# Kernel optimization log

Measured on AMD Instinct MI355X. Metric: run time of the kernel, lower is better.

Reference implementation:

```python
import jax, jax.numpy as jnp
import numpy as np

EPS = 1e-12  # matches torch.nn.functional.normalize default eps


def _l2norm(x, axis=-1):
    # F.normalize: x / max(||x||, eps)
    n = jnp.sqrt(jnp.sum(x * x, axis=axis, keepdims=True))
    return x / jnp.maximum(n, EPS)


def setup_inputs() -> dict:
    key = jax.random.key(0)
    k1, k2, k3 = jax.random.split(key, 3)
    batch, n_mels, time_steps = 32, 80, 4000
    num_codebooks, codebook_size, d = 2, 1024, 64
    mel = jax.random.normal(k1, (batch, n_mels, time_steps), dtype=jnp.float32)
    proj = jax.random.normal(k2, (num_codebooks, n_mels, d), dtype=jnp.float32)
    codebooks = jax.random.normal(k3, (num_codebooks, codebook_size, d), dtype=jnp.float32)
    return {"mel": mel, "proj": proj, "codebooks": codebooks}


def reference(mel, proj, codebooks):
    # mel: [b, n, t] -> [b, t, n]
    mel_t = jnp.transpose(mel, (0, 2, 1))
    # project for all codebooks at once: [c, b, t, d]
    p = jnp.einsum('btn,cnd->cbtd', mel_t, proj)
    p = _l2norm(p, axis=-1)
    cb = _l2norm(codebooks, axis=-1)  # [c, k, d]
    # cosine similarity: [c, b, t, k]
    sim = jnp.einsum('cbtd,ckd->cbtk', p, cb)
    codes = jnp.argmax(sim, axis=-1)  # [c, b, t]
    return codes
```

## Files before the change

kernel.cpp:

```cpp
#include <hip/hip_runtime.h>
#include <hip/hip_bf16.h>
#include <math.h>
#include <stdint.h>


#define B      32
#define NMELS  80
#define TSTEPS 4000
#define NCB    2
#define KCB    1024
#define DDIM   64
#define TPB    256
#define TM     64
#define KT     32
#define NKT    (KCB / KT)
#define PPAD   66

typedef short bf16x8 __attribute__((ext_vector_type(8)));
typedef float f32x4  __attribute__((ext_vector_type(4)));

#define WS_CB_OFF   8192
#define WS_NEEDED   (8192 + NCB*KCB*DDIM*2)

static __device__ __forceinline__ uint32_t bits(float f) {
    return __builtin_bit_cast(uint32_t, f);
}
static __device__ __forceinline__ float fbits(uint32_t u) {
    return __builtin_bit_cast(float, u);
}
static __device__ __forceinline__ uint32_t rne16(uint32_t u) {
    return (u + 0x7FFFu + ((u >> 16) & 1u)) >> 16;
}

__global__ __launch_bounds__(TPB) void rpq_prep(const float* __restrict__ cb,
                                                float* __restrict__ ws)
{
    const int idx = blockIdx.x * TPB + threadIdx.x;
    if (idx >= NCB * KCB) return;

    const float4* row = (const float4*)(cb + (size_t)idx * DDIM);
    float4 v[16];
    float ss = 0.f;
    #pragma unroll
    for (int i = 0; i < 16; ++i) {
        v[i] = row[i];
        ss += v[i].x*v[i].x + v[i].y*v[i].y + v[i].z*v[i].z + v[i].w*v[i].w;
    }
    const float inv = 1.0f / fmaxf(sqrtf(ss), 1e-12f);
    ws[idx] = inv;

    uint32_t dw[32];
    #pragma unroll
    for (int i = 0; i < 16; ++i) {
        dw[2*i]   = rne16(bits(v[i].x * inv)) | (rne16(bits(v[i].y * inv)) << 16);
        dw[2*i+1] = rne16(bits(v[i].z * inv)) | (rne16(bits(v[i].w * inv)) << 16);
    }
    uint4* dst = (uint4*)((char*)ws + WS_CB_OFF + (size_t)idx * 128);
    #pragma unroll
    for (int i = 0; i < 8; ++i)
        dst[i] = make_uint4(dw[4*i], dw[4*i+1], dw[4*i+2], dw[4*i+3]);
}

__global__ __launch_bounds__(TPB, 5) void rpq_main(
    const float* __restrict__ mel,
    const float* __restrict__ proj,
    const float* __restrict__ cb,
    const float* __restrict__ ws,
    int* __restrict__ out)
{
    const int tid  = threadIdx.x;
    const int b    = blockIdx.y;
    const int c    = blockIdx.z;
    const int t0   = blockIdx.x * TM;

    const int l    = tid & 63;
    const int wid  = tid >> 6;
    const int lrow = l & 15;
    const int lgrp = l >> 4;

    __shared__ union __align__(16) {
        float projS[NMELS * DDIM];
        struct {
            union {
                char     cbuf[2][KT * 128];
                uint32_t candT[16][TM][2];
            } a;
            float PL[TM * PPAD];
            float scv[TM][9];
            int   sck[TM][9];
        } p2;
    } U;

    const char*  wscb   = (const char*)ws + WS_CB_OFF + (size_t)c * (KCB * 128);
    const float* invn_g = ws + (size_t)c * KCB;

    {
        const float4* src = (const float4*)(proj + (size_t)c * NMELS * DDIM);
        float4* dst = (float4*)U.projS;
        for (int i = tid; i < NMELS * DDIM / 4; i += TPB) dst[i] = src[i];
    }
    __syncthreads();

    const int srow = tid >> 3;
    const int sq   = tid & 7;
    uint4 g0;
    g0 = *(const uint4*)(wscb + (size_t)tid * 16);

    {
        const int tq = tid & 15;
        const int dg = tid >> 4;
        const int tbase  = t0 + tq * 4;
        const int tb_c   = (tbase <= TSTEPS - 4) ? tbase : (TSTEPS - 4);
        const float* mp  = mel + (size_t)b * NMELS * TSTEPS + tb_c;

        float Pa[4][4];
        #pragma unroll
        for (int i = 0; i < 4; ++i)
            #pragma unroll
            for (int j = 0; j < 4; ++j) Pa[i][j] = 0.f;

        for (int n = 0; n < NMELS; ++n) {
            const float4 m4 = *(const float4*)(mp + (size_t)n * TSTEPS);
            const float4 w  = *(const float4*)&U.projS[n * DDIM + dg * 4];
            Pa[0][0] = fmaf(m4.x, w.x, Pa[0][0]); Pa[0][1] = fmaf(m4.x, w.y, Pa[0][1]);
            Pa[0][2] = fmaf(m4.x, w.z, Pa[0][2]); Pa[0][3] = fmaf(m4.x, w.w, Pa[0][3]);
            Pa[1][0] = fmaf(m4.y, w.x, Pa[1][0]); Pa[1][1] = fmaf(m4.y, w.y, Pa[1][1]);
            Pa[1][2] = fmaf(m4.y, w.z, Pa[1][2]); Pa[1][3] = fmaf(m4.y, w.w, Pa[1][3]);
            Pa[2][0] = fmaf(m4.z, w.x, Pa[2][0]); Pa[2][1] = fmaf(m4.z, w.y, Pa[2][1]);
            Pa[2][2] = fmaf(m4.z, w.z, Pa[2][2]); Pa[2][3] = fmaf(m4.z, w.w, Pa[2][3]);
            Pa[3][0] = fmaf(m4.w, w.x, Pa[3][0]); Pa[3][1] = fmaf(m4.w, w.y, Pa[3][1]);
            Pa[3][2] = fmaf(m4.w, w.z, Pa[3][2]); Pa[3][3] = fmaf(m4.w, w.w, Pa[3][3]);
        }
        __syncthreads();

        #pragma unroll
        for (int i = 0; i < 4; ++i)
            *(float4*)&U.p2.PL[(tq * 4 + i) * PPAD + dg * 4] =
                make_float4(Pa[i][0], Pa[i][1], Pa[i][2], Pa[i][3]);
    }

    {
        const int xw = (srow & 7) << 4;
        *(uint4*)(&U.p2.a.cbuf[0][srow * 128] + ((sq * 16) ^ xw)) = g0;
    }
    __syncthreads();

    bf16x8 A0, A1;
    {
        const float* pr = &U.p2.PL[((wid << 4) + lrow) * PPAD];
        #pragma unroll
        for (int i = 0; i < 8; ++i) {
            A0[i] = (short)rne16(bits(pr[lgrp * 8 + i]));
            A1[i] = (short)rne16(bits(pr[32 + lgrp * 8 + i]));
        }
    }

    float m1[4], m2[4];
    #pragma unroll
    for (int r = 0; r < 4; ++r) { m1[r] = -INFINITY; m2[r] = -INFINITY; }
    uint32_t idxv = (uint32_t)(1023 - lrow);

    const int xr  = (lrow & 7) << 4;
    const int bo0 = (lgrp * 16) ^ xr;
    const int bo1 = (64 + lgrp * 16) ^ xr;

    for (int kt = 0; kt < NKT; ++kt) {
        const int cur = kt & 1;
        if (kt + 1 < NKT) {
            g0 = *(const uint4*)(wscb + (size_t)(kt + 1) * (KT * 128)
                                 + (size_t)tid * 16);
        }
        const char* buf = U.p2.a.cbuf[cur];
        #pragma unroll
        for (int s = 0; s < 2; ++s) {
            const char* rowp = buf + (s * 16 + lrow) * 128;
            bf16x8 B0 = *(const bf16x8*)(rowp + bo0);
            bf16x8 B1 = *(const bf16x8*)(rowp + bo1);
            f32x4 acc = {0.f, 0.f, 0.f, 0.f};
            acc = __builtin_amdgcn_mfma_f32_16x16x32_bf16(A0, B0, acc, 0, 0, 0);
            acc = __builtin_amdgcn_mfma_f32_16x16x32_bf16(A1, B1, acc, 0, 0, 0);
            #pragma unroll
            for (int r = 0; r < 4; ++r) {
                const float pf = fbits((bits(acc[r]) & 0xFFFFFC00u)
                                     | (idxv & 0x3FFu));
                m2[r] = __builtin_amdgcn_fmed3f(pf, m1[r], m2[r]);
                m1[r] = fmaxf(pf, m1[r]);
            }
            idxv -= 16u;
        }
        if (kt + 1 < NKT) {
            const int xw = (srow & 7) << 4;
            *(uint4*)(&U.p2.a.cbuf[cur ^ 1][srow * 128] + ((sq * 16) ^ xw)) = g0;
        }
        __syncthreads();
    }

    #pragma unroll
    for (int r = 0; r < 4; ++r) {
        const int trow = (wid << 4) + (lgrp << 2) + r;
        U.p2.a.candT[lrow][trow][0] = bits(m1[r]);
        U.p2.a.candT[lrow][trow][1] = bits(m2[r]);
    }
    __syncthreads();

    {
        const int t = tid & 63;
        const int j = wid;
        float c1 = -INFINITY, c2 = -INFINITY, c3 = -INFINITY, c4 = -INFINITY;
        float c5 = -INFINITY, c6 = -INFINITY, c7 = -INFINITY, c8 = -INFINITY;
        for (int i = 0; i < 16; ++i) {
            const uint2 pv2 = *(const uint2*)&U.p2.a.candT[i][t][0];
            #pragma unroll
            for (int jj = 0; jj < 2; ++jj) {
                const float p = fbits(jj ? pv2.y : pv2.x);
                c8 = fmaxf(fminf(p, c7), c8);
                c7 = fmaxf(fminf(p, c6), c7);
                c6 = fmaxf(fminf(p, c5), c6);
                c5 = fmaxf(fminf(p, c4), c5);
                c4 = fmaxf(fminf(p, c3), c4);
                c3 = fmaxf(fminf(p, c2), c3);
                c2 = fmaxf(fminf(p, c1), c2);
                c1 = fmaxf(p, c1);
            }
        }
        const float sel0 = (j == 0) ? c1 : (j == 1) ? c3 : (j == 2) ? c5 : c7;
        const float sel1 = (j == 0) ? c2 : (j == 1) ? c4 : (j == 2) ? c6 : c8;
        const float* pr  = &U.p2.PL[t * PPAD];
        const float* cbc = cb + (size_t)c * KCB * DDIM;
        #pragma unroll
        for (int e = 0; e < 2; ++e) {
            const float sel = e ? sel1 : sel0;
            const int kj = 1023 - (int)(bits(sel) & 0x3FFu);
            const float* cbr = cbc + (size_t)kj * DDIM;
            float a0 = 0.f, a1 = 0.f, a2 = 0.f, a3 = 0.f;
            #pragma unroll
            for (int i = 0; i < 16; ++i) {
                float4 pv = *(const float4*)(pr + i * 4);
                float4 cv = *(const float4*)(cbr + i * 4);
                a0 = fmaf(pv.x, cv.x, a0); a1 = fmaf(pv.y, cv.y, a1);
                a2 = fmaf(pv.z, cv.z, a2); a3 = fmaf(pv.w, cv.w, a3);
            }
            U.p2.scv[t][2*j + e] = ((a0 + a1) + (a2 + a3)) * invn_g[kj];
            U.p2.sck[t][2*j + e] = kj;
        }
    }
    __syncthreads();

    if (tid < TM) {
        const int tg = t0 + tid;
        if (tg < TSTEPS) {
            float best = U.p2.scv[tid][0];
            int   bk   = U.p2.sck[tid][0];
            #pragma unroll
            for (int s2 = 1; s2 < 8; ++s2) {
                const float v = U.p2.scv[tid][s2];
                const int  kk = U.p2.sck[tid][s2];
                if (v > best || (v == best && kk < bk)) { best = v; bk = kk; }
            }
            out[((size_t)c * B + b) * TSTEPS + tg] = bk;
        }
    }
}

__global__ __launch_bounds__(TPB, 2) void rpq_fallback(
    const float* __restrict__ mel, const float* __restrict__ proj,
    const float* __restrict__ cb, int* __restrict__ out)
{
    const int tid = threadIdx.x;
    const int b = blockIdx.y, c = blockIdx.z;
    const int t0 = blockIdx.x * (TPB * 2) + tid;
    const int t1 = t0 + TPB;
    const int tc0 = (t0 < TSTEPS) ? t0 : (TSTEPS - 1);
    const int tc1 = (t1 < TSTEPS) ? t1 : (TSTEPS - 1);

    __shared__ union { float projS[NMELS*DDIM]; float cbS[2][64*DDIM]; } sh;
    __shared__ float invn[KCB];
    const float* cbc = cb + (size_t)c * KCB * DDIM;
    {
        const float4* src = (const float4*)(proj + (size_t)c * NMELS * DDIM);
        float4* dst = (float4*)sh.projS;
        for (int i = tid; i < NMELS*DDIM/4; i += TPB) dst[i] = src[i];
    }
    for (int j = 0; j < KCB/TPB; ++j) {
        const int k = j*TPB + tid;
        const float4* r = (const float4*)(cbc + (size_t)k * DDIM);
        float s = 0.f;
        #pragma unroll
        for (int i = 0; i < DDIM/4; ++i) {
            float4 v = r[i]; s += v.x*v.x + v.y*v.y + v.z*v.z + v.w*v.w;
        }
        invn[k] = 1.0f / fmaxf(sqrtf(s), 1e-12f);
    }
    float4 r0, r1, r2, r3;
    { const float4* g = (const float4*)cbc;
      r0 = g[tid]; r1 = g[tid+256]; r2 = g[tid+512]; r3 = g[tid+768]; }
    __syncthreads();
    float P0[DDIM], P1[DDIM];
    #pragma unroll
    for (int d = 0; d < DDIM; ++d) { P0[d] = 0.f; P1[d] = 0.f; }
    const float* mp = mel + (size_t)b * NMELS * TSTEPS;
    for (int n = 0; n < NMELS; ++n) {
        const float m0 = mp[(size_t)n*TSTEPS + tc0];
        const float m1_ = mp[(size_t)n*TSTEPS + tc1];
        const float4* ps = (const float4*)(sh.projS + n*DDIM);
        #pragma unroll
        for (int i = 0; i < DDIM/4; ++i) {
            float4 v = ps[i];
            P0[4*i+0]=fmaf(m0,v.x,P0[4*i+0]); P0[4*i+1]=fmaf(m0,v.y,P0[4*i+1]);
            P0[4*i+2]=fmaf(m0,v.z,P0[4*i+2]); P0[4*i+3]=fmaf(m0,v.w,P0[4*i+3]);
            P1[4*i+0]=fmaf(m1_,v.x,P1[4*i+0]); P1[4*i+1]=fmaf(m1_,v.y,P1[4*i+1]);
            P1[4*i+2]=fmaf(m1_,v.z,P1[4*i+2]); P1[4*i+3]=fmaf(m1_,v.w,P1[4*i+3]);
        }
    }
    __syncthreads();
    { float4* dst = (float4*)sh.cbS[0];
      dst[tid]=r0; dst[tid+256]=r1; dst[tid+512]=r2; dst[tid+768]=r3; }
    { const float4* g = (const float4*)(cbc + (size_t)64*DDIM);
      r0=g[tid]; r1=g[tid+256]; r2=g[tid+512]; r3=g[tid+768]; }
    __syncthreads();
    float best0 = -INFINITY, best1 = -INFINITY; int bi0 = 0, bi1 = 0;
    for (int kt = 0; kt < KCB/64; ++kt) {
        const int cur = kt & 1;
        const float* base = sh.cbS[cur];
        const int kbase = kt * 64;
        #pragma unroll 2
        for (int kk = 0; kk < 64; ++kk) {
            const float4* row = (const float4*)(base + kk*DDIM);
            float a0=0,a1=0,a2=0,a3=0,b0=0,b1=0,b2=0,b3=0;
            #pragma unroll
            for (int i = 0; i < DDIM/4; ++i) {
                float4 v = row[i];
                a0=fmaf(P0[4*i+0],v.x,a0); a1=fmaf(P0[4*i+1],v.y,a1);
                a2=fmaf(P0[4*i+2],v.z,a2); a3=fmaf(P0[4*i+3],v.w,a3);
                b0=fmaf(P1[4*i+0],v.x,b0); b1=fmaf(P1[4*i+1],v.y,b1);
                b2=fmaf(P1[4*i+2],v.z,b2); b3=fmaf(P1[4*i+3],v.w,b3);
            }
            const int k = kbase + kk;
            const float w = invn[k];
            const float s0 = ((a0+a1)+(a2+a3))*w;
            const float s1 = ((b0+b1)+(b2+b3))*w;
            if (s0 > best0) { best0 = s0; bi0 = k; }
            if (s1 > best1) { best1 = s1; bi1 = k; }
        }
        if (kt + 1 < KCB/64) {
            float4* dst = (float4*)sh.cbS[cur ^ 1];
            dst[tid]=r0; dst[tid+256]=r1; dst[tid+512]=r2; dst[tid+768]=r3;
            if (kt + 2 < KCB/64) {
                const float4* g = (const float4*)(cbc + (size_t)(kt+2)*64*DDIM);
                r0=g[tid]; r1=g[tid+256]; r2=g[tid+512]; r3=g[tid+768];
            }
        }
        __syncthreads();
    }
    const size_t ob = ((size_t)c * B + b) * TSTEPS;
    if (t0 < TSTEPS) out[ob + t0] = bi0;
    if (t1 < TSTEPS) out[ob + t1] = bi1;
}

extern "C" void kernel_launch(void* const* d_in, const int* in_sizes, int n_in,
                              void* d_out, int out_size, void* d_ws, size_t ws_size,
                              hipStream_t stream) {
    const float* mel  = (const float*)d_in[0];
    const float* proj = (const float*)d_in[1];
    const float* cb   = (const float*)d_in[2];
    int* out = (int*)d_out;

    if (ws_size >= (size_t)WS_NEEDED) {
        float* ws = (float*)d_ws;
        rpq_prep<<<dim3((NCB*KCB + TPB - 1)/TPB), dim3(TPB), 0, stream>>>(cb, ws);
        dim3 grid((TSTEPS + TM - 1) / TM, B, NCB);
        rpq_main<<<grid, dim3(TPB), 0, stream>>>(mel, proj, cb, ws, out);
    } else {
        dim3 grid((TSTEPS + TPB*2 - 1) / (TPB*2), B, NCB);
        rpq_fallback<<<grid, dim3(TPB), 0, stream>>>(mel, proj, cb, out);
    }
}
```

Measured before the change: 193.1 us.

## Split codebook across waves, reading B directly from global without LDS staging

Each wave now processes all 64 time rows against its own quarter of the codebook (256 entries), loading bf16 codebook fragments straight from global/L2 instead of double-buffering them through LDS with a block barrier every tile. Per-lane top-2 candidates are merged with xor-shuffles within the wave and written once per wave, replacing the 16-way shared-memory candidate transpose and the serial top-8 insertion. This removes the per-tile __syncthreads and LDS traffic and reuses each B fragment across four A tiles. In exchange it raises register pressure (4 A tiles, 16 m1/m2 pairs), so occupancy drops to 4 blocks, and B loads now depend on global latency.

```diff
diff --git a/kernel.cpp b/kernel.cpp
--- a/kernel.cpp
+++ b/kernel.cpp
@@ -12,8 +12,6 @@
 #define DDIM   64
 #define TPB    256
 #define TM     64
-#define KT     32
-#define NKT    (KCB / KT)
 #define PPAD   66
 
 typedef short bf16x8 __attribute__((ext_vector_type(8)));
@@ -61,7 +59,7 @@
         dst[i] = make_uint4(dw[4*i], dw[4*i+1], dw[4*i+2], dw[4*i+3]);
 }
 
-__global__ __launch_bounds__(TPB, 5) void rpq_main(
+__global__ __launch_bounds__(TPB, 4) void rpq_main(
     const float* __restrict__ mel,
     const float* __restrict__ proj,
     const float* __restrict__ cb,
@@ -81,11 +79,8 @@
     __shared__ union __align__(16) {
         float projS[NMELS * DDIM];
         struct {
-            union {
-                char     cbuf[2][KT * 128];
-                uint32_t candT[16][TM][2];
-            } a;
             float PL[TM * PPAD];
+            uint2 wcand[4][TM];
             float scv[TM][9];
             int   sck[TM][9];
         } p2;
@@ -100,11 +95,6 @@
         for (int i = tid; i < NMELS * DDIM / 4; i += TPB) dst[i] = src[i];
     }
     __syncthreads();
-
-    const int srow = tid >> 3;
-    const int sq   = tid & 7;
-    uint4 g0;
-    g0 = *(const uint4*)(wscb + (size_t)tid * 16);
 
     {
         const int tq = tid & 15;
@@ -138,99 +128,80 @@
             *(float4*)&U.p2.PL[(tq * 4 + i) * PPAD + dg * 4] =
                 make_float4(Pa[i][0], Pa[i][1], Pa[i][2], Pa[i][3]);
     }
-
-    {
-        const int xw = (srow & 7) << 4;
-        *(uint4*)(&U.p2.a.cbuf[0][srow * 128] + ((sq * 16) ^ xw)) = g0;
-    }
-    __syncthreads();
-
-    bf16x8 A0, A1;
-    {
-        const float* pr = &U.p2.PL[((wid << 4) + lrow) * PPAD];
+    __syncthreads();
+
+    bf16x8 A0[4], A1[4];
+    #pragma unroll
+    for (int tb = 0; tb < 4; ++tb) {
+        const float* pr = &U.p2.PL[(tb * 16 + lrow) * PPAD];
         #pragma unroll
         for (int i = 0; i < 8; ++i) {
-            A0[i] = (short)rne16(bits(pr[lgrp * 8 + i]));
-            A1[i] = (short)rne16(bits(pr[32 + lgrp * 8 + i]));
-        }
-    }
-
-    float m1[4], m2[4];
-    #pragma unroll
-    for (int r = 0; r < 4; ++r) { m1[r] = -INFINITY; m2[r] = -INFINITY; }
-    uint32_t idxv = (uint32_t)(1023 - lrow);
-
-    const int xr  = (lrow & 7) << 4;
-    const int bo0 = (lgrp * 16) ^ xr;
-    const int bo1 = (64 + lgrp * 16) ^ xr;
-
-    for (int kt = 0; kt < NKT; ++kt) {
-        const int cur = kt & 1;
-        if (kt + 1 < NKT) {
-            g0 = *(const uint4*)(wscb + (size_t)(kt + 1) * (KT * 128)
-                                 + (size_t)tid * 16);
-        }
-        const char* buf = U.p2.a.cbuf[cur];
-        #pragma unroll
-        for (int s = 0; s < 2; ++s) {
-            const char* rowp = buf + (s * 16 + lrow) * 128;
-            bf16x8 B0 = *(const bf16x8*)(rowp + bo0);
-            bf16x8 B1 = *(const bf16x8*)(rowp + bo1);
+            A0[tb][i] = (short)rne16(bits(pr[lgrp * 8 + i]));
+            A1[tb][i] = (short)rne16(bits(pr[32 + lgrp * 8 + i]));
+        }
+    }
+
+    float m1[4][4], m2[4][4];
+    #pragma unroll
+    for (int tb = 0; tb < 4; ++tb)
+        #pragma unroll
+        for (int r = 0; r < 4; ++r) { m1[tb][r] = -INFINITY; m2[tb][r] = -INFINITY; }
+
+    const char* qbase = wscb + (size_t)wid * (256 * 128);
+    const int lo0 = lrow * 128 + lgrp * 16;
+    const int lo1 = lo0 + 64;
+    uint32_t idxv = (uint32_t)(1023 - (wid << 8) - lrow);
+
+    #pragma unroll 4
+    for (int g = 0; g < 16; ++g) {
+        const bf16x8 B0 = *(const bf16x8*)(qbase + g * 2048 + lo0);
+        const bf16x8 B1 = *(const bf16x8*)(qbase + g * 2048 + lo1);
+        #pragma unroll
+        for (int tb = 0; tb < 4; ++tb) {
             f32x4 acc = {0.f, 0.f, 0.f, 0.f};
-            acc = __builtin_amdgcn_mfma_f32_16x16x32_bf16(A0, B0, acc, 0, 0, 0);
-            acc = __builtin_amdgcn_mfma_f32_16x16x32_bf16(A1, B1, acc, 0, 0, 0);
+            acc = __builtin_amdgcn_mfma_f32_16x16x32_bf16(A0[tb], B0, acc, 0, 0, 0);
+            acc = __builtin_amdgcn_mfma_f32_16x16x32_bf16(A1[tb], B1, acc, 0, 0, 0);
             #pragma unroll
             for (int r = 0; r < 4; ++r) {
                 const float pf = fbits((bits(acc[r]) & 0xFFFFFC00u)
                                      | (idxv & 0x3FFu));
-                m2[r] = __builtin_amdgcn_fmed3f(pf, m1[r], m2[r]);
-                m1[r] = fmaxf(pf, m1[r]);
-            }
-            idxv -= 16u;
-        }
-        if (kt + 1 < NKT) {
-            const int xw = (srow & 7) << 4;
-            *(uint4*)(&U.p2.a.cbuf[cur ^ 1][srow * 128] + ((sq * 16) ^ xw)) = g0;
-        }
-        __syncthreads();
-    }
-
-    #pragma unroll
-    for (int r = 0; r < 4; ++r) {
-        const int trow = (wid << 4) + (lgrp << 2) + r;
-        U.p2.a.candT[lrow][trow][0] = bits(m1[r]);
-        U.p2.a.candT[lrow][trow][1] = bits(m2[r]);
+                m2[tb][r] = __builtin_amdgcn_fmed3f(pf, m1[tb][r], m2[tb][r]);
+                m1[tb][r] = fmaxf(pf, m1[tb][r]);
+            }
+        }
+        idxv -= 16u;
+    }
+
+    #pragma unroll
+    for (int tb = 0; tb < 4; ++tb) {
+        #pragma unroll
+        for (int r = 0; r < 4; ++r) {
+            float a1 = m1[tb][r], a2 = m2[tb][r];
+            #pragma unroll
+            for (int m = 1; m <= 8; m <<= 1) {
+                const float b1 = __shfl_xor(a1, m);
+                const float b2 = __shfl_xor(a2, m);
+                const float lo = fminf(a1, b1);
+                a1 = fmaxf(a1, b1);
+                a2 = fmaxf(lo, fmaxf(a2, b2));
+            }
+            if (lrow == 0)
+                U.p2.wcand[wid][tb * 16 + (lgrp << 2) + r] =
+                    make_uint2(bits(a1), bits(a2));
+        }
     }
     __syncthreads();
 
     {
         const int t = tid & 63;
         const int j = wid;
-        float c1 = -INFINITY, c2 = -INFINITY, c3 = -INFINITY, c4 = -INFINITY;
-        float c5 = -INFINITY, c6 = -INFINITY, c7 = -INFINITY, c8 = -INFINITY;
-        for (int i = 0; i < 16; ++i) {
-            const uint2 pv2 = *(const uint2*)&U.p2.a.candT[i][t][0];
-            #pragma unroll
-            for (int jj = 0; jj < 2; ++jj) {
-                const float p = fbits(jj ? pv2.y : pv2.x);
-                c8 = fmaxf(fminf(p, c7), c8);
-                c7 = fmaxf(fminf(p, c6), c7);
-                c6 = fmaxf(fminf(p, c5), c6);
-                c5 = fmaxf(fminf(p, c4), c5);
-                c4 = fmaxf(fminf(p, c3), c4);
-                c3 = fmaxf(fminf(p, c2), c3);
-                c2 = fmaxf(fminf(p, c1), c2);
-                c1 = fmaxf(p, c1);
-            }
-        }
-        const float sel0 = (j == 0) ? c1 : (j == 1) ? c3 : (j == 2) ? c5 : c7;
-        const float sel1 = (j == 0) ? c2 : (j == 1) ? c4 : (j == 2) ? c6 : c8;
+        const uint2 cd = U.p2.wcand[j][t];
         const float* pr  = &U.p2.PL[t * PPAD];
         const float* cbc = cb + (size_t)c * KCB * DDIM;
         #pragma unroll
         for (int e = 0; e < 2; ++e) {
-            const float sel = e ? sel1 : sel0;
-            const int kj = 1023 - (int)(bits(sel) & 0x3FFu);
+            const uint32_t sv = e ? cd.y : cd.x;
+            const int kj = 1023 - (int)(sv & 0x3FFu);
             const float* cbr = cbc + (size_t)kj * DDIM;
             float a0 = 0.f, a1 = 0.f, a2 = 0.f, a3 = 0.f;
             #pragma unroll
```

Result: faster. 177.9 us (-7.9%).

## Stream bf16 codebook directly from global memory with smaller wave-local blocks

Applied to the files above, without the earlier changes.

The main kernel drops LDS staging of both the projection matrix and the bf16 codebook tiles. Projection weights are read straight from global memory, and each wave loads its MFMA B operands from the prepped workspace with no per-tile barriers. Blocks shrink to 128 threads covering 32 time steps with higher occupancy bounds, and candidate reduction becomes per-wave. This removes LDS traffic and __syncthreads in the codebook loop, but relies on L1/L2 caching for repeated codebook and projection reads across many more blocks.

```diff
diff --git a/kernel.cpp b/kernel.cpp
--- a/kernel.cpp
+++ b/kernel.cpp
@@ -10,10 +10,8 @@
 #define NCB    2
 #define KCB    1024
 #define DDIM   64
-#define TPB    256
-#define TM     64
-#define KT     32
-#define NKT    (KCB / KT)
+#define TPB    128
+#define TM     32
 #define PPAD   66
 
 typedef short bf16x8 __attribute__((ext_vector_type(8)));
@@ -32,10 +30,10 @@
     return (u + 0x7FFFu + ((u >> 16) & 1u)) >> 16;
 }
 
-__global__ __launch_bounds__(TPB) void rpq_prep(const float* __restrict__ cb,
+__global__ __launch_bounds__(256) void rpq_prep(const float* __restrict__ cb,
                                                 float* __restrict__ ws)
 {
-    const int idx = blockIdx.x * TPB + threadIdx.x;
+    const int idx = blockIdx.x * 256 + threadIdx.x;
     if (idx >= NCB * KCB) return;
 
     const float4* row = (const float4*)(cb + (size_t)idx * DDIM);
@@ -61,7 +59,7 @@
         dst[i] = make_uint4(dw[4*i], dw[4*i+1], dw[4*i+2], dw[4*i+3]);
 }
 
-__global__ __launch_bounds__(TPB, 5) void rpq_main(
+__global__ __launch_bounds__(TPB, 8) void rpq_main(
     const float* __restrict__ mel,
     const float* __restrict__ proj,
     const float* __restrict__ cb,
@@ -74,44 +72,25 @@
     const int t0   = blockIdx.x * TM;
 
     const int l    = tid & 63;
-    const int wid  = tid >> 6;
+    const int w    = tid >> 6;
     const int lrow = l & 15;
     const int lgrp = l >> 4;
 
-    __shared__ union __align__(16) {
-        float projS[NMELS * DDIM];
-        struct {
-            union {
-                char     cbuf[2][KT * 128];
-                uint32_t candT[16][TM][2];
-            } a;
-            float PL[TM * PPAD];
-            float scv[TM][9];
-            int   sck[TM][9];
-        } p2;
-    } U;
+    __shared__ struct __align__(16) {
+        float    PL[TM * PPAD];
+        uint2    cand[2][16][17];
+        float    scv[2][16][9];
+        int      sck[2][16][9];
+    } S;
 
     const char*  wscb   = (const char*)ws + WS_CB_OFF + (size_t)c * (KCB * 128);
     const float* invn_g = ws + (size_t)c * KCB;
 
     {
-        const float4* src = (const float4*)(proj + (size_t)c * NMELS * DDIM);
-        float4* dst = (float4*)U.projS;
-        for (int i = tid; i < NMELS * DDIM / 4; i += TPB) dst[i] = src[i];
-    }
-    __syncthreads();
-
-    const int srow = tid >> 3;
-    const int sq   = tid & 7;
-    uint4 g0;
-    g0 = *(const uint4*)(wscb + (size_t)tid * 16);
-
-    {
-        const int tq = tid & 15;
-        const int dg = tid >> 4;
-        const int tbase  = t0 + tq * 4;
-        const int tb_c   = (tbase <= TSTEPS - 4) ? tbase : (TSTEPS - 4);
-        const float* mp  = mel + (size_t)b * NMELS * TSTEPS + tb_c;
+        const int tq = tid & 7;
+        const int dg = tid >> 3;
+        const float* mp = mel + (size_t)b * NMELS * TSTEPS + t0 + tq * 4;
+        const float* pj = proj + (size_t)c * NMELS * DDIM + dg * 4;
 
         float Pa[4][4];
         #pragma unroll
@@ -121,33 +100,26 @@
 
         for (int n = 0; n < NMELS; ++n) {
             const float4 m4 = *(const float4*)(mp + (size_t)n * TSTEPS);
-            const float4 w  = *(const float4*)&U.projS[n * DDIM + dg * 4];
-            Pa[0][0] = fmaf(m4.x, w.x, Pa[0][0]); Pa[0][1] = fmaf(m4.x, w.y, Pa[0][1]);
-            Pa[0][2] = fmaf(m4.x, w.z, Pa[0][2]); Pa[0][3] = fmaf(m4.x, w.w, Pa[0][3]);
-            Pa[1][0] = fmaf(m4.y, w.x, Pa[1][0]); Pa[1][1] = fmaf(m4.y, w.y, Pa[1][1]);
-            Pa[1][2] = fmaf(m4.y, w.z, Pa[1][2]); Pa[1][3] = fmaf(m4.y, w.w, Pa[1][3]);
-            Pa[2][0] = fmaf(m4.z, w.x, Pa[2][0]); Pa[2][1] = fmaf(m4.z, w.y, Pa[2][1]);
-            Pa[2][2] = fmaf(m4.z, w.z, Pa[2][2]); Pa[2][3] = fmaf(m4.z, w.w, Pa[2][3]);
-            Pa[3][0] = fmaf(m4.w, w.x, Pa[3][0]); Pa[3][1] = fmaf(m4.w, w.y, Pa[3][1]);
-            Pa[3][2] = fmaf(m4.w, w.z, Pa[3][2]); Pa[3][3] = fmaf(m4.w, w.w, Pa[3][3]);
-        }
-        __syncthreads();
-
+            const float4 wv = *(const float4*)(pj + (size_t)n * DDIM);
+            Pa[0][0] = fmaf(m4.x, wv.x, Pa[0][0]); Pa[0][1] = fmaf(m4.x, wv.y, Pa[0][1]);
+            Pa[0][2] = fmaf(m4.x, wv.z, Pa[0][2]); Pa[0][3] = fmaf(m4.x, wv.w, Pa[0][3]);
+            Pa[1][0] = fmaf(m4.y, wv.x, Pa[1][0]); Pa[1][1] = fmaf(m4.y, wv.y, Pa[1][1]);
+            Pa[1][2] = fmaf(m4.y, wv.z, Pa[1][2]); Pa[1][3] = fmaf(m4.y, wv.w, Pa[1][3]);
+            Pa[2][0] = fmaf(m4.z, wv.x, Pa[2][0]); Pa[2][1] = fmaf(m4.z, wv.y, Pa[2][1]);
+            Pa[2][2] = fmaf(m4.z, wv.z, Pa[2][2]); Pa[2][3] = fmaf(m4.z, wv.w, Pa[2][3]);
+            Pa[3][0] = fmaf(m4.w, wv.x, Pa[3][0]); Pa[3][1] = fmaf(m4.w, wv.y, Pa[3][1]);
+            Pa[3][2] = fmaf(m4.w, wv.z, Pa[3][2]); Pa[3][3] = fmaf(m4.w, wv.w, Pa[3][3]);
+        }
         #pragma unroll
         for (int i = 0; i < 4; ++i)
-            *(float4*)&U.p2.PL[(tq * 4 + i) * PPAD + dg * 4] =
+            *(float4*)&S.PL[(tq * 4 + i) * PPAD + dg * 4] =
                 make_float4(Pa[i][0], Pa[i][1], Pa[i][2], Pa[i][3]);
-    }
-
-    {
-        const int xw = (srow & 7) << 4;
-        *(uint4*)(&U.p2.a.cbuf[0][srow * 128] + ((sq * 16) ^ xw)) = g0;
     }
     __syncthreads();
 
     bf16x8 A0, A1;
     {
-        const float* pr = &U.p2.PL[((wid << 4) + lrow) * PPAD];
+        const float* pr = &S.PL[(w * 16 + lrow) * PPAD];
         #pragma unroll
         for (int i = 0; i < 8; ++i) {
             A0[i] = (short)rne16(bits(pr[lgrp * 8 + i]));
@@ -158,58 +130,39 @@
     float m1[4], m2[4];
     #pragma unroll
     for (int r = 0; r < 4; ++r) { m1[r] = -INFINITY; m2[r] = -INFINITY; }
+
+    const int lo0 = lrow * 128 + lgrp * 16;
+    const int lo1 = lo0 + 64;
     uint32_t idxv = (uint32_t)(1023 - lrow);
 
-    const int xr  = (lrow & 7) << 4;
-    const int bo0 = (lgrp * 16) ^ xr;
-    const int bo1 = (64 + lgrp * 16) ^ xr;
-
-    for (int kt = 0; kt < NKT; ++kt) {
-        const int cur = kt & 1;
-        if (kt + 1 < NKT) {
-            g0 = *(const uint4*)(wscb + (size_t)(kt + 1) * (KT * 128)
-                                 + (size_t)tid * 16);
-        }
-        const char* buf = U.p2.a.cbuf[cur];
-        #pragma unroll
-        for (int s = 0; s < 2; ++s) {
-            const char* rowp = buf + (s * 16 + lrow) * 128;
-            bf16x8 B0 = *(const bf16x8*)(rowp + bo0);
-            bf16x8 B1 = *(const bf16x8*)(rowp + bo1);
-            f32x4 acc = {0.f, 0.f, 0.f, 0.f};
-            acc = __builtin_amdgcn_mfma_f32_16x16x32_bf16(A0, B0, acc, 0, 0, 0);
-            acc = __builtin_amdgcn_mfma_f32_16x16x32_bf16(A1, B1, acc, 0, 0, 0);
-            #pragma unroll
-            for (int r = 0; r < 4; ++r) {
-                const float pf = fbits((bits(acc[r]) & 0xFFFFFC00u)
-                                     | (idxv & 0x3FFu));
-                m2[r] = __builtin_amdgcn_fmed3f(pf, m1[r], m2[r]);
-                m1[r] = fmaxf(pf, m1[r]);
-            }
-            idxv -= 16u;
-        }
-        if (kt + 1 < NKT) {
-            const int xw = (srow & 7) << 4;
-            *(uint4*)(&U.p2.a.cbuf[cur ^ 1][srow * 128] + ((sq * 16) ^ xw)) = g0;
-        }
-        __syncthreads();
-    }
-
-    #pragma unroll
-    for (int r = 0; r < 4; ++r) {
-        const int trow = (wid << 4) + (lgrp << 2) + r;
-        U.p2.a.candT[lrow][trow][0] = bits(m1[r]);
-        U.p2.a.candT[lrow][trow][1] = bits(m2[r]);
-    }
+    #pragma unroll 4
+    for (int g = 0; g < 64; ++g) {
+        const bf16x8 B0 = *(const bf16x8*)(wscb + (size_t)g * 2048 + lo0);
+        const bf16x8 B1 = *(const bf16x8*)(wscb + (size_t)g * 2048 + lo1);
+        f32x4 acc = {0.f, 0.f, 0.f, 0.f};
+        acc = __builtin_amdgcn_mfma_f32_16x16x32_bf16(A0, B0, acc, 0, 0, 0);
+        acc = __builtin_amdgcn_mfma_f32_16x16x32_bf16(A1, B1, acc, 0, 0, 0);
+        #pragma unroll
+        for (int r = 0; r < 4; ++r) {
+            const float pf = fbits((bits(acc[r]) & 0xFFFFFC00u) | (idxv & 0x3FFu));
+            m2[r] = __builtin_amdgcn_fmed3f(pf, m1[r], m2[r]);
+            m1[r] = fmaxf(pf, m1[r]);
+        }
+        idxv -= 16u;
+    }
+
+    #pragma unroll
+    for (int r = 0; r < 4; ++r)
+        S.cand[w][(lgrp << 2) + r][lrow] = make_uint2(bits(m1[r]), bits(m2[r]));
     __syncthreads();
 
     {
-        const int t = tid & 63;
-        const int j = wid;
+        const int t = l & 15;
+        const int j = lgrp;
         float c1 = -INFINITY, c2 = -INFINITY, c3 = -INFINITY, c4 = -INFINITY;
         float c5 = -INFINITY, c6 = -INFINITY, c7 = -INFINITY, c8 = -INFINITY;
         for (int i = 0; i < 16; ++i) {
-            const uint2 pv2 = *(const uint2*)&U.p2.a.candT[i][t][0];
+            const uint2 pv2 = S.cand[w][t][i];
             #pragma unroll
             for (int jj = 0; jj < 2; ++jj) {
                 const float p = fbits(jj ? pv2.y : pv2.x);
@@ -225,7 +178,7 @@
         }
         const float sel0 = (j == 0) ? c1 : (j == 1) ? c3 : (j == 2) ? c5 : c7;
         const float sel1 = (j == 0) ? c2 : (j == 1) ? c4 : (j == 2) ? c6 : c8;
-        const float* pr  = &U.p2.PL[t * PPAD];
+        const float* pr  = &S.PL[(w * 16 + t) * PPAD];
         const float* cbc = cb + (size_t)c * KCB * DDIM;
         #pragma unroll
         for (int e = 0; e < 2; ++e) {
@@ -240,36 +193,35 @@
                 a0 = fmaf(pv.x, cv.x, a0); a1 = fmaf(pv.y, cv.y, a1);
                 a2 = fmaf(pv.z, cv.z, a2); a3 = fmaf(pv.w, cv.w, a3);
             }
-            U.p2.scv[t][2*j + e] = ((a0 + a1) + (a2 + a3)) * invn_g[kj];
-            U.p2.sck[t][2*j + e] = kj;
-        }
-    }
-    __syncthreads();
-
-    if (tid < TM) {
-        const int tg = t0 + tid;
-        if (tg < TSTEPS) {
-            float best = U.p2.scv[tid][0];
-            int   bk   = U.p2.sck[tid][0];
-            #pragma unroll
-            for (int s2 = 1; s2 < 8; ++s2) {
-                const float v = U.p2.scv[tid][s2];
-                const int  kk = U.p2.sck[tid][s2];
-                if (v > best || (v == best && kk < bk)) { best = v; bk = kk; }
-            }
-            out[((size_t)c * B + b) * TSTEPS + tg] = bk;
-        }
-    }
-}
-
-__global__ __launch_bounds__(TPB, 2) void rpq_fallback(
+            S.scv[w][t][2*j + e] = ((a0 + a1) + (a2 + a3)) * invn_g[kj];
+            S.sck[w][t][2*j + e] = kj;
+        }
+    }
+    __syncthreads();
+
+    if (l < 16) {
+        const int tg = t0 + w * 16 + l;
+        float best = S.scv[w][l][0];
+        int   bk   = S.sck[w][l][0];
+        #pragma unroll
+        for (int s2 = 1; s2 < 8; ++s2) {
+            const float v = S.scv[w][l][s2];
+            const int  kk = S.sck[w][l][s2];
+            if (v > best || (v == best && kk < bk)) { best = v; bk = kk; }
+        }
+        out[((size_t)c * B + b) * TSTEPS + tg] = bk;
+    }
+}
+
+#define FTPB 256
+__global__ __launch_bounds__(FTPB, 2) void rpq_fallback(
     const float* __restrict__ mel, const float* __restrict__ proj,
     const float* __restrict__ cb, int* __restrict__ out)
 {
     const int tid = threadIdx.x;
     const int b = blockIdx.y, c = blockIdx.z;
-    const int t0 = blockIdx.x * (TPB * 2) + tid;
-    const int t1 = t0 + TPB;
+    const int t0 = blockIdx.x * (FTPB * 2) + tid;
+    const int t1 = t0 + FTPB;
     const int tc0 = (t0 < TSTEPS) ? t0 : (TSTEPS - 1);
     const int tc1 = (t1 < TSTEPS) ? t1 : (TSTEPS - 1);
 
@@ -279,10 +231,10 @@
     {
         const float4* src = (const float4*)(proj + (size_t)c * NMELS * DDIM);
         float4* dst = (float4*)sh.projS;
-        for (int i = tid; i < NMELS*DDIM/4; i += TPB) dst[i] = src[i];
-    }
-    for (int j = 0; j < KCB/TPB; ++j) {
-        const int k = j*TPB + tid;
+        for (int i = tid; i < NMELS*DDIM/4; i += FTPB) dst[i] = src[i];
+    }
+    for (int j = 0; j < KCB/FTPB; ++j) {
+        const int k = j*FTPB + tid;
         const float4* r = (const float4*)(cbc + (size_t)k * DDIM);
         float s = 0.f;
         #pragma unroll
@@ -336,9 +288,9 @@
                 b2=fmaf(P1[4*i+2],v.z,b2); b3=fmaf(P1[4*i+3],v.w,b3);
             }
             const int k = kbase + kk;
-            const float w = invn[k];
-            const float s0 = ((a0+a1)+(a2+a3))*w;
-            const float s1 = ((b0+b1)+(b2+b3))*w;
+            const float wv = invn[k];
+            const float s0 = ((a0+a1)+(a2+a3))*wv;
+            const float s1 = ((b0+b1)+(b2+b3))*wv;
             if (s0 > best0) { best0 = s0; bi0 = k; }
             if (s1 > best1) { best1 = s1; bi1 = k; }
         }
@@ -367,11 +319,11 @@
 
     if (ws_size >= (size_t)WS_NEEDED) {
         float* ws = (float*)d_ws;
-        rpq_prep<<<dim3((NCB*KCB + TPB - 1)/TPB), dim3(TPB), 0, stream>>>(cb, ws);
-        dim3 grid((TSTEPS + TM - 1) / TM, B, NCB);
+        rpq_prep<<<dim3((NCB*KCB + 255)/256), dim3(256), 0, stream>>>(cb, ws);
+        dim3 grid(TSTEPS / TM, B, NCB);
         rpq_main<<<grid, dim3(TPB), 0, stream>>>(mel, proj, cb, ws, out);
     } else {
-        dim3 grid((TSTEPS + TPB*2 - 1) / (TPB*2), B, NCB);
-        rpq_fallback<<<grid, dim3(TPB), 0, stream>>>(mel, proj, cb, out);
-    }
-}
+        dim3 grid((TSTEPS + FTPB*2 - 1) / (FTPB*2), B, NCB);
+        rpq_fallback<<<grid, dim3(FTPB), 0, stream>>>(mel, proj, cb, out);
+    }
+}
```

After: 365.2 us. 1.89x slower.

## Prefetch codebook tiles two ahead, alias rescoring scratch, raise occupancy target

Applied to the files above, without the earlier changes.

Codebook tiles now stream through two register slots that load two iterations ahead, so global latency has more time to hide behind the MFMA loop, which is unrolled by two. The rescoring scratch arrays are moved into the union with the candidate buffer, with an extra barrier between the top-8 selection and the rescoring. This cuts LDS use so the launch bound can rise to 6 blocks per CU. The risks are register pressure from the extra prefetch slot under a tighter register cap, and one more block-wide sync.

```diff
diff --git a/kernel.cpp b/kernel.cpp
--- a/kernel.cpp
+++ b/kernel.cpp
@@ -61,7 +61,7 @@
         dst[i] = make_uint4(dw[4*i], dw[4*i+1], dw[4*i+2], dw[4*i+3]);
 }
 
-__global__ __launch_bounds__(TPB, 5) void rpq_main(
+__global__ __launch_bounds__(TPB, 6) void rpq_main(
     const float* __restrict__ mel,
     const float* __restrict__ proj,
     const float* __restrict__ cb,
@@ -84,10 +84,12 @@
             union {
                 char     cbuf[2][KT * 128];
                 uint32_t candT[16][TM][2];
+                struct {
+                    float scv[TM][9];
+                    int   sck[TM][9];
+                } m;
             } a;
             float PL[TM * PPAD];
-            float scv[TM][9];
-            int   sck[TM][9];
         } p2;
     } U;
 
@@ -103,8 +105,9 @@
 
     const int srow = tid >> 3;
     const int sq   = tid & 7;
-    uint4 g0;
-    g0 = *(const uint4*)(wscb + (size_t)tid * 16);
+    uint4 ga, gb;
+    ga = *(const uint4*)(wscb + (size_t)tid * 16);
+    gb = *(const uint4*)(wscb + (size_t)KT * 128 + (size_t)tid * 16);
 
     {
         const int tq = tid & 15;
@@ -139,9 +142,10 @@
                 make_float4(Pa[i][0], Pa[i][1], Pa[i][2], Pa[i][3]);
     }
 
-    {
-        const int xw = (srow & 7) << 4;
-        *(uint4*)(&U.p2.a.cbuf[0][srow * 128] + ((sq * 16) ^ xw)) = g0;
+    const int xw = (srow & 7) << 4;
+    {
+        *(uint4*)(&U.p2.a.cbuf[0][srow * 128] + ((sq * 16) ^ xw)) = ga;
+        ga = *(const uint4*)(wscb + (size_t)2 * (KT * 128) + (size_t)tid * 16);
     }
     __syncthreads();
 
@@ -164,13 +168,9 @@
     const int bo0 = (lgrp * 16) ^ xr;
     const int bo1 = (64 + lgrp * 16) ^ xr;
 
+    #pragma unroll 2
     for (int kt = 0; kt < NKT; ++kt) {
-        const int cur = kt & 1;
-        if (kt + 1 < NKT) {
-            g0 = *(const uint4*)(wscb + (size_t)(kt + 1) * (KT * 128)
-                                 + (size_t)tid * 16);
-        }
-        const char* buf = U.p2.a.cbuf[cur];
+        const char* buf = U.p2.a.cbuf[kt & 1];
         #pragma unroll
         for (int s = 0; s < 2; ++s) {
             const char* rowp = buf + (s * 16 + lrow) * 128;
@@ -189,8 +189,18 @@
             idxv -= 16u;
         }
         if (kt + 1 < NKT) {
-            const int xw = (srow & 7) << 4;
-            *(uint4*)(&U.p2.a.cbuf[cur ^ 1][srow * 128] + ((sq * 16) ^ xw)) = g0;
+            char* base = &U.p2.a.cbuf[(kt + 1) & 1][srow * 128];
+            if ((kt + 1) & 1) {
+                *(uint4*)(base + ((sq * 16) ^ xw)) = gb;
+                if (kt + 3 < NKT)
+                    gb = *(const uint4*)(wscb + (size_t)(kt + 3) * (KT * 128)
+                                         + (size_t)tid * 16);
+            } else {
+                *(uint4*)(base + ((sq * 16) ^ xw)) = ga;
+                if (kt + 3 < NKT)
+                    ga = *(const uint4*)(wscb + (size_t)(kt + 3) * (KT * 128)
+                                         + (size_t)tid * 16);
+            }
         }
         __syncthreads();
     }
@@ -203,6 +213,7 @@
     }
     __syncthreads();
 
+    float sel0, sel1;
     {
         const int t = tid & 63;
         const int j = wid;
@@ -223,8 +234,14 @@
                 c1 = fmaxf(p, c1);
             }
         }
-        const float sel0 = (j == 0) ? c1 : (j == 1) ? c3 : (j == 2) ? c5 : c7;
-        const float sel1 = (j == 0) ? c2 : (j == 1) ? c4 : (j == 2) ? c6 : c8;
+        sel0 = (j == 0) ? c1 : (j == 1) ? c3 : (j == 2) ? c5 : c7;
+        sel1 = (j == 0) ? c2 : (j == 1) ? c4 : (j == 2) ? c6 : c8;
+    }
+    __syncthreads();
+
+    {
+        const int t = tid & 63;
+        const int j = wid;
         const float* pr  = &U.p2.PL[t * PPAD];
         const float* cbc = cb + (size_t)c * KCB * DDIM;
         #pragma unroll
@@ -240,8 +257,8 @@
                 a0 = fmaf(pv.x, cv.x, a0); a1 = fmaf(pv.y, cv.y, a1);
                 a2 = fmaf(pv.z, cv.z, a2); a3 = fmaf(pv.w, cv.w, a3);
             }
-            U.p2.scv[t][2*j + e] = ((a0 + a1) + (a2 + a3)) * invn_g[kj];
-            U.p2.sck[t][2*j + e] = kj;
+            U.p2.a.m.scv[t][2*j + e] = ((a0 + a1) + (a2 + a3)) * invn_g[kj];
+            U.p2.a.m.sck[t][2*j + e] = kj;
         }
     }
     __syncthreads();
@@ -249,12 +266,12 @@
     if (tid < TM) {
         const int tg = t0 + tid;
         if (tg < TSTEPS) {
-            float best = U.p2.scv[tid][0];
-            int   bk   = U.p2.sck[tid][0];
+            float best = U.p2.a.m.scv[tid][0];
+            int   bk   = U.p2.a.m.sck[tid][0];
             #pragma unroll
             for (int s2 = 1; s2 < 8; ++s2) {
-                const float v = U.p2.scv[tid][s2];
-                const int  kk = U.p2.sck[tid][s2];
+                const float v = U.p2.a.m.scv[tid][s2];
+                const int  kk = U.p2.a.m.sck[tid][s2];
                 if (v > best || (v == best && kk < bk)) { best = v; bk = kk; }
             }
             out[((size_t)c * B + b) * TSTEPS + tg] = bk;
```

After: 191.1 us. No clear change (-1.0%).
